# Kernel optimization log

Measured on AMD Instinct MI355X. Metric: run time of the kernel, lower is better.

The kernel has to match this reference:

```python
import jax, jax.numpy as jnp
import numpy as np
from jax import lax

EPS = 1e-5

def conv1x1(x, w, b=None):
    # x: [B,C,H,W], w: [O,C]
    y = jnp.einsum('bchw,oc->bohw', x, w)
    if b is not None:
        y = y + b[None, :, None, None]
    return y

def channel_attention(x, w1, w2):
    # x: [B,C,H,W]; w1: [C//r, C]; w2: [C, C//r]
    avg = jnp.mean(x, axis=(2, 3))                     # [B,C]
    h = jax.nn.relu(jnp.einsum('bc,rc->br', avg, w1))  # [B,C//r]
    s = jax.nn.sigmoid(jnp.einsum('br,cr->bc', h, w2)) # [B,C]
    return s[:, :, None, None]

def spatial_attention(x, w, b):
    # x: [B,C,H,W]; w: [1,2,7,7]
    avg = jnp.mean(x, axis=1, keepdims=True)
    mx = jnp.max(x, axis=1, keepdims=True)
    cat = jnp.concatenate([avg, mx], axis=1)           # [B,2,H,W]
    y = lax.conv_general_dilated(cat, w, (1, 1), 'SAME',
                                 dimension_numbers=('NCHW', 'OIHW', 'NCHW'))
    return jax.nn.sigmoid(y + b[None, :, None, None])

def cross_attention(x, y, q_w, q_b, k_w, k_b, v_w, v_b, gamma):
    B, C, H, W = x.shape
    HW = H * W
    q = conv1x1(x, q_w, q_b).reshape(B, -1, HW)        # [B,C8,HW]
    k = conv1x1(y, k_w, k_b).reshape(B, -1, HW)        # [B,C8,HW]
    v = conv1x1(y, v_w, v_b).reshape(B, C, HW)         # [B,C,HW]
    attn = jax.nn.softmax(jnp.einsum('bcn,bcm->bnm', q, k), axis=-1)  # [B,HW,HW]
    out = jnp.einsum('bcm,bnm->bcn', v, attn).reshape(B, C, H, W)
    return gamma * out + x

def batchnorm_relu(x, scale, bias):
    # train-mode BN: batch statistics over (N,H,W)
    mean = jnp.mean(x, axis=(0, 2, 3), keepdims=True)
    var = jnp.var(x, axis=(0, 2, 3), keepdims=True)
    xn = (x - mean) * lax.rsqrt(var + EPS)
    return jax.nn.relu(xn * scale[None, :, None, None] + bias[None, :, None, None])

def caf_forward(swin_feat, resnet_feat, proj_w, proj_b, ca_w1, ca_w2, sa_w, sa_b,
                q_w, q_b, k_w, k_b, v_w, v_b, gamma, refine_w, refine_b, bn_scale, bn_bias):
    s = conv1x1(swin_feat, proj_w, proj_b)
    r = conv1x1(resnet_feat, proj_w, proj_b)
    es = s * channel_attention(s, ca_w1, ca_w2) * spatial_attention(s, sa_w, sa_b)
    er = r * channel_attention(r, ca_w1, ca_w2) * spatial_attention(r, sa_w, sa_b)
    cross = cross_attention(es, er, q_w, q_b, k_w, k_b, v_w, v_b, gamma)
    cat = jnp.concatenate([cross, es], axis=1)         # [B, 2C, H, W]
    y = conv1x1(cat, refine_w, refine_b)
    return batchnorm_relu(y, bn_scale, bn_bias)

def setup_inputs() -> dict:
    key = jax.random.key(0)
    ks = jax.random.split(key, 16)
    B, Cin, H, W = 4, 128, 64, 64
    C = 64            # resnet_ch // 2
    R = C // 16       # channel attention reduction
    C8 = C // 8       # cross-attention qk dim
    sd = lambda fan_in: 1.0 / np.sqrt(fan_in)
    return {
        'swin_feat': jax.random.normal(ks[0], (B, Cin, H, W), jnp.float32),
        'resnet_feat': jax.random.normal(ks[1], (B, Cin, H, W), jnp.float32),
        'proj_w': jax.random.normal(ks[2], (C, Cin), jnp.float32) * sd(Cin),
        'proj_b': jnp.zeros((C,), jnp.float32),
        'ca_w1': jax.random.normal(ks[3], (R, C), jnp.float32) * sd(C),
        'ca_w2': jax.random.normal(ks[4], (C, R), jnp.float32) * sd(R),
        'sa_w': jax.random.normal(ks[5], (1, 2, 7, 7), jnp.float32) * sd(2 * 49),
        'sa_b': jnp.zeros((1,), jnp.float32),
        'q_w': jax.random.normal(ks[6], (C8, C), jnp.float32) * sd(C),
        'q_b': jnp.zeros((C8,), jnp.float32),
        'k_w': jax.random.normal(ks[7], (C8, C), jnp.float32) * sd(C),
        'k_b': jnp.zeros((C8,), jnp.float32),
        'v_w': jax.random.normal(ks[8], (C, C), jnp.float32) * sd(C),
        'v_b': jnp.zeros((C,), jnp.float32),
        'gamma': jnp.zeros((1,), jnp.float32),
        'refine_w': jax.random.normal(ks[9], (2 * C, 2 * C), jnp.float32) * sd(2 * C),
        'refine_b': jnp.zeros((2 * C,), jnp.float32),
        'bn_scale': jnp.ones((2 * C,), jnp.float32),
        'bn_bias': jnp.zeros((2 * C,), jnp.float32),
    }

def reference(swin_feat, resnet_feat, proj_w, proj_b, ca_w1, ca_w2, sa_w, sa_b,
              q_w, q_b, k_w, k_b, v_w, v_b, gamma, refine_w, refine_b, bn_scale, bn_bias):
    return caf_forward(swin_feat, resnet_feat, proj_w, proj_b, ca_w1, ca_w2, sa_w, sa_b,
                       q_w, q_b, k_w, k_b, v_w, v_b, gamma, refine_w, refine_b, bn_scale, bn_bias)
```

## Files before the change

### kernel.cpp

```cpp
#include <hip/hip_runtime.h>
#include <hip/hip_bf16.h>
#include <math.h>

#define NB   4
#define CIN  128
#define C    64
#define HH   64
#define WW   64
#define HW   4096
#define C8   8
#define RR   4
#define TWOC 128
#define LOG2E 1.44269504088896340736f

typedef __attribute__((ext_vector_type(8))) short short8;
typedef __attribute__((ext_vector_type(4))) float f32x4;
typedef __attribute__((ext_vector_type(16))) float f32x16;
typedef __attribute__((ext_vector_type(4))) int int4v;
typedef __attribute__((ext_vector_type(2))) unsigned uint2v;

__device__ inline ushort f2bf(float f) {
    union { float f; unsigned u; } x{ f };
    unsigned r = x.u + 0x7FFFu + ((x.u >> 16) & 1u);
    return (ushort)(r >> 16);
}

__device__ inline float fexp2(float x) { return __builtin_amdgcn_exp2f(x); }

__device__ inline short8 cvt8(f32x4 a, f32x4 b) {
    union { int i[4]; short8 s; } u;
    asm("v_cvt_pk_bf16_f32 %0, %1, %2" : "=v"(u.i[0]) : "v"(a[0]), "v"(a[1]));
    asm("v_cvt_pk_bf16_f32 %0, %1, %2" : "=v"(u.i[1]) : "v"(a[2]), "v"(a[3]));
    asm("v_cvt_pk_bf16_f32 %0, %1, %2" : "=v"(u.i[2]) : "v"(b[0]), "v"(b[1]));
    asm("v_cvt_pk_bf16_f32 %0, %1, %2" : "=v"(u.i[3]) : "v"(b[2]), "v"(b[3]));
    return u.s;
}

__global__ __launch_bounds__(256) void proj_gemm_kernel(
    const float* __restrict__ sw, const float* __restrict__ rn,
    const float* __restrict__ w, const float* __restrict__ bias,
    const float* __restrict__ gammap,
    float* __restrict__ s_t, float* __restrict__ r_t,
    float* __restrict__ part, float* __restrict__ avgc, float* __restrict__ maxc) {
    int bid = blockIdx.x;
    int hwT = bid & 63;
    int b   = (bid >> 6) & 3;
    int img = bid >> 8;
    if (img == 1 && gammap[0] == 0.f) return;
    int hw0 = hwT << 6;
    const float* x = (img ? rn : sw) + (size_t)b * CIN * HW + hw0;
    float* y = (img ? r_t : s_t) + (size_t)b * HW * C;

    __shared__ ushort xt[64 * 132];
    __shared__ float redc[4][64];
    int t = threadIdx.x;
    {
        int hwl = t & 63, cq = t >> 6;
        #pragma unroll
        for (int i = 0; i < 16; ++i) {
            int c = cq * 32 + i * 2;
            float a  = x[(size_t)c * HW + hwl];
            float b2 = x[(size_t)(c + 1) * HW + hwl];
            int pk;
            asm("v_cvt_pk_bf16_f32 %0, %1, %2" : "=v"(pk) : "v"(a), "v"(b2));
            *(unsigned*)&xt[hwl * 132 + c] = (unsigned)pk;
        }
    }
    __syncthreads();

    int lane = t & 63, wv = t >> 6;
    int colL = lane & 15, g = lane >> 4;
    int hwsub = wv << 4;
    f32x4 acc[4] = {};
    #pragma unroll
    for (int ks = 0; ks < 4; ++ks) {
        const ushort* ap = &xt[(hwsub + colL) * 132 + ks * 32 + g * 8];
        union { uint2 u2[2]; short8 s; } af;
        af.u2[0] = *(const uint2*)ap;
        af.u2[1] = *(const uint2*)(ap + 4);
        #pragma unroll
        for (int ot = 0; ot < 4; ++ot) {
            const float* wp = w + (size_t)(ot * 16 + colL) * CIN + ks * 32 + g * 8;
            short8 bf = cvt8(*(const f32x4*)wp, *(const f32x4*)(wp + 4));
            acc[ot] = __builtin_amdgcn_mfma_f32_16x16x32_bf16(af.s, bf, acc[ot], 0, 0, 0);
        }
    }

    float rowsum[4], rowmax[4], colsum[4];
    #pragma unroll
    for (int r = 0; r < 4; ++r) { rowsum[r] = 0.f; rowmax[r] = -1e30f; }
    #pragma unroll
    for (int ot = 0; ot < 4; ++ot) colsum[ot] = 0.f;
    #pragma unroll
    for (int ot = 0; ot < 4; ++ot) {
        float bb = bias[ot * 16 + colL];
        #pragma unroll
        for (int r = 0; r < 4; ++r) {
            float v = acc[ot][r] + bb;
            y[(size_t)(hw0 + hwsub + g * 4 + r) * C + ot * 16 + colL] = v;
            rowsum[r] += v;
            rowmax[r] = fmaxf(rowmax[r], v);
            colsum[ot] += v;
        }
    }
    #pragma unroll
    for (int d = 1; d < 16; d <<= 1) {
        #pragma unroll
        for (int r = 0; r < 4; ++r) {
            rowsum[r] += __shfl_xor(rowsum[r], d);
            rowmax[r] = fmaxf(rowmax[r], __shfl_xor(rowmax[r], d));
        }
    }
    if (colL == 0) {
        int ob = (img * 4 + b) * HW + hw0 + hwsub + g * 4;
        #pragma unroll
        for (int r = 0; r < 4; ++r) {
            avgc[ob + r] = rowsum[r] * (1.f / C);
            maxc[ob + r] = rowmax[r];
        }
    }
    #pragma unroll
    for (int d = 16; d < 64; d <<= 1) {
        #pragma unroll
        for (int ot = 0; ot < 4; ++ot) colsum[ot] += __shfl_xor(colsum[ot], d);
    }
    if (g == 0) {
        #pragma unroll
        for (int ot = 0; ot < 4; ++ot) redc[wv][ot * 16 + colL] = colsum[ot];
    }
    __syncthreads();
    if (t < 64)
        part[((size_t)(img * 4 + b) * 64 + hwT) * 64 + t] =
            redc[0][t] + redc[1][t] + redc[2][t] + redc[3][t];
}

__global__ __launch_bounds__(256) void casa_kernel(
    const float* __restrict__ part, const float* __restrict__ w1,
    const float* __restrict__ w2, float* __restrict__ cab,
    const float* __restrict__ avgc, const float* __restrict__ maxc,
    const float* __restrict__ saw, const float* __restrict__ bsa,
    const float* __restrict__ gammap, float* __restrict__ sab) {
    int bid = blockIdx.x;
    int t = threadIdx.x;
    if (bid == 128) {
        __shared__ float avs[8][64];
        __shared__ float hsh[8][RR];
        #pragma unroll
        for (int it = 0; it < 2; ++it) {
            int idx = t + it * 256;
            int c = idx & 63, ib = idx >> 6;
            float avg = 0.f;
            for (int hwT = 0; hwT < 64; ++hwT)
                avg += part[((size_t)ib * 64 + hwT) * 64 + c];
            avs[ib][c] = avg * (1.f / HW);
        }
        __syncthreads();
        if (t < 32) {
            int ib2 = t >> 2, r = t & 3;
            float a = 0.f;
            for (int cc = 0; cc < C; ++cc) a += avs[ib2][cc] * w1[r * C + cc];
            hsh[ib2][r] = fmaxf(a, 0.f);
        }
        __syncthreads();
        #pragma unroll
        for (int it = 0; it < 2; ++it) {
            int idx = t + it * 256;
            int c = idx & 63, ib = idx >> 6;
            float a = 0.f;
            #pragma unroll
            for (int r = 0; r < RR; ++r) a += hsh[ib][r] * w2[c * RR + r];
            cab[ib * 64 + c] = 1.f / (1.f + __expf(-a));
        }
        return;
    }
    int img = bid >> 6;
    if (img == 1 && gammap[0] == 0.f) return;
    __shared__ float wsh[98];
    if (t < 98) wsh[t] = saw[t];
    __syncthreads();
    int idx = (bid & 63) * 256 + t;
    int b = idx >> 12, hw = idx & 4095;
    int base = (img * 4 + b) * HW;
    int y0 = hw >> 6, x0 = hw & 63;
    float acc = bsa[0];
    for (int dy = -3; dy <= 3; ++dy) {
        int yy = y0 + dy; if (yy < 0 || yy >= HH) continue;
        for (int dx = -3; dx <= 3; ++dx) {
            int xx = x0 + dx; if (xx < 0 || xx >= WW) continue;
            int widx = (dy + 3) * 7 + (dx + 3);
            int p = base + yy * WW + xx;
            acc += avgc[p] * wsh[widx] + maxc[p] * wsh[49 + widx];
        }
    }
    sab[base + hw] = 1.f / (1.f + __expf(-acc));
}

__global__ __launch_bounds__(256) void vqk_proj_kernel(
    const float* __restrict__ es, const float* __restrict__ er,
    const float* __restrict__ vw, const float* __restrict__ vbv,
    const float* __restrict__ qw, const float* __restrict__ qbv,
    const float* __restrict__ kw, const float* __restrict__ kbv,
    const float* __restrict__ gammap,
    const float* __restrict__ cab, const float* __restrict__ sab,
    ushort* __restrict__ v_t, ushort* __restrict__ q_t, ushort* __restrict__ k_t) {
    if (gammap[0] == 0.f) return;
    __shared__ float wsh[64][64];
    __shared__ float qsh[8][64], ksh[8][64];
    int t = threadIdx.x;
    for (int i = t; i < 4096; i += 256) wsh[i >> 6][i & 63] = vw[i];
    for (int i = t; i < 512; i += 256) qsh[i >> 6][i & 63] = qw[i];
    for (int i = t; i < 512; i += 256) ksh[i >> 6][i & 63] = kw[i];
    __syncthreads();

    int bid = blockIdx.x;
    int hw = ((bid & 63) << 6) + (t & 63);
    int b  = bid >> 6;
    int qt = t >> 6;
    int c0 = qt << 4;
    const float* erp = er + (size_t)(b * HW + hw) * C;
    const float* esp = es + (size_t)(b * HW + hw) * C;
    const float* cas = cab + b * 64;
    const float* car = cab + (4 + b) * 64;
    float gs = sab[b * HW + hw];
    float gr = sab[(4 + b) * HW + hw];

    float va[16];
    #pragma unroll
    for (int j = 0; j < 16; ++j) va[j] = vbv[c0 + j];
    float qa[8], ka[8];
    #pragma unroll
    for (int o = 0; o < 8; ++o) { qa[o] = qbv[o]; ka[o] = kbv[o]; }

    #pragma unroll 4
    for (int i = 0; i < 16; ++i) {
        f32x4 xr = *(const f32x4*)(erp + i * 4) * *(const f32x4*)(car + i * 4) * gr;
        #pragma unroll
        for (int j = 0; j < 16; ++j) {
            const float* wr = &wsh[c0 + j][i * 4];
            va[j] += xr[0]*wr[0] + xr[1]*wr[1] + xr[2]*wr[2] + xr[3]*wr[3];
        }
        if (qt == 0) {
            f32x4 xs = *(const f32x4*)(esp + i * 4) * *(const f32x4*)(cas + i * 4) * gs;
            #pragma unroll
            for (int o = 0; o < 8; ++o) {
                const float* wr = &qsh[o][i * 4];
                qa[o] += xs[0]*wr[0] + xs[1]*wr[1] + xs[2]*wr[2] + xs[3]*wr[3];
            }
        } else if (qt == 3) {
            #pragma unroll
            for (int o = 0; o < 8; ++o) {
                const float* wr = &ksh[o][i * 4];
                ka[o] += xr[0]*wr[0] + xr[1]*wr[1] + xr[2]*wr[2] + xr[3]*wr[3];
            }
        }
    }

    #pragma unroll
    for (int j = 0; j < 16; ++j)
        v_t[((size_t)(b * C + c0 + j) << 12) + hw] = f2bf(va[j]);
    if (qt == 0) {
        union { ushort u[8]; int4v v; } qo;
        #pragma unroll
        for (int o = 0; o < 8; ++o) qo.u[o] = f2bf(qa[o] * LOG2E);
        *(int4v*)(q_t + (size_t)(b * HW + hw) * 8) = qo.v;
    } else if (qt == 3) {
        union { ushort u[8]; int4v v; } ko;
        #pragma unroll
        for (int o = 0; o < 8; ++o) ko.u[o] = f2bf(ka[o]);
        *(int4v*)(k_t + (size_t)(b * HW + hw) * 8) = ko.v;
    }
}

__global__ __launch_bounds__(512) void cross_attn_mfma(
    const ushort* __restrict__ q_t, const ushort* __restrict__ k_t,
    const ushort* __restrict__ v_t, const float* __restrict__ es_t,
    const float* __restrict__ gammap,
    const float* __restrict__ cab, const float* __restrict__ sab,
    float* __restrict__ cross_t)
{
    const float gma = gammap[0];
    if (gma == 0.f) return;
    const int tid  = threadIdx.x;
    const int lane = tid & 63;
    const int ws   = tid >> 6;
    const int b    = blockIdx.x >> 7;
    const int n0   = (blockIdx.x & 127) << 5;
    const int l31  = lane & 31;
    const int h    = lane >> 5;

    short8 qf = short8(0);
    if (lane < 32) qf = *(const short8*)(q_t + ((size_t)(b * HW) + n0 + l31) * 8);

    f32x16 acc0 = (f32x16)(0.f), acc1 = (f32x16)(0.f);
    float mrun = -1e30f, lrun = 0.f;

    const ushort* kbase = k_t + (size_t)(b * HW) * 8;
    const ushort* vb0 = v_t + ((size_t)(b * C) + l31) * HW + 8 * h;
    const ushort* vb1 = v_t + ((size_t)(b * C) + 32 + l31) * HW + 8 * h;

    const int mbeg = ws << 9, mend = mbeg + 512;
    for (int m0 = mbeg; m0 < mend; m0 += 32) {
        short8 kf = short8(0);
        if (lane < 32) kf = *(const short8*)(kbase + ((size_t)(m0 + l31)) * 8);
        short8 v00 = *(const short8*)(vb0 + m0);
        short8 v01 = *(const short8*)(vb0 + m0 + 16);
        short8 v10 = *(const short8*)(vb1 + m0);
        short8 v11 = *(const short8*)(vb1 + m0 + 16);

        f32x16 s = __builtin_amdgcn_mfma_f32_32x32x16_bf16(kf, qf, (f32x16)(0.f), 0, 0, 0);

        float t0 = fmaxf(fmaxf(s[0], s[1]), fmaxf(s[2], s[3]));
        float t1 = fmaxf(fmaxf(s[4], s[5]), fmaxf(s[6], s[7]));
        float t2 = fmaxf(fmaxf(s[8], s[9]), fmaxf(s[10], s[11]));
        float t3 = fmaxf(fmaxf(s[12], s[13]), fmaxf(s[14], s[15]));
        float tmax = fmaxf(fmaxf(t0, t1), fmaxf(t2, t3));
        tmax = fmaxf(tmax, __shfl_xor(tmax, 32));

        if (!__all(tmax <= mrun)) {
            float mnew = fmaxf(mrun, tmax);
            float corr = fexp2(mrun - mnew);
            lrun *= corr;
            acc0 *= corr;
            acc1 *= corr;
            mrun = mnew;
        }

        float p[16];
        #pragma unroll
        for (int r = 0; r < 16; ++r) p[r] = fexp2(s[r] - mrun);
        float ts = ((p[0]+p[1]) + (p[2]+p[3])) + ((p[4]+p[5]) + (p[6]+p[7]))
                 + ((p[8]+p[9]) + (p[10]+p[11])) + ((p[12]+p[13]) + (p[14]+p[15]));
        ts += __shfl_xor(ts, 32);
        lrun += ts;

        int c01, c23, c45, c67, c89, cAB, cCD, cEF;
        asm("v_cvt_pk_bf16_f32 %0, %1, %2" : "=v"(c01) : "v"(p[0]),  "v"(p[1]));
        asm("v_cvt_pk_bf16_f32 %0, %1, %2" : "=v"(c23) : "v"(p[2]),  "v"(p[3]));
        asm("v_cvt_pk_bf16_f32 %0, %1, %2" : "=v"(c45) : "v"(p[4]),  "v"(p[5]));
        asm("v_cvt_pk_bf16_f32 %0, %1, %2" : "=v"(c67) : "v"(p[6]),  "v"(p[7]));
        asm("v_cvt_pk_bf16_f32 %0, %1, %2" : "=v"(c89) : "v"(p[8]),  "v"(p[9]));
        asm("v_cvt_pk_bf16_f32 %0, %1, %2" : "=v"(cAB) : "v"(p[10]), "v"(p[11]));
        asm("v_cvt_pk_bf16_f32 %0, %1, %2" : "=v"(cCD) : "v"(p[12]), "v"(p[13]));
        asm("v_cvt_pk_bf16_f32 %0, %1, %2" : "=v"(cEF) : "v"(p[14]), "v"(p[15]));

        uint2v s1 = __builtin_amdgcn_permlane32_swap(c45, c01, false, false);
        uint2v s2 = __builtin_amdgcn_permlane32_swap(c67, c23, false, false);
        uint2v s3 = __builtin_amdgcn_permlane32_swap(cCD, c89, false, false);
        uint2v s4 = __builtin_amdgcn_permlane32_swap(cEF, cAB, false, false);

        union { unsigned u[4]; short8 s; } B0, B1;
        B0.u[0] = s1[1]; B0.u[1] = s2[1]; B0.u[2] = s1[0]; B0.u[3] = s2[0];
        B1.u[0] = s3[1]; B1.u[1] = s4[1]; B1.u[2] = s3[0]; B1.u[3] = s4[0];

        acc0 = __builtin_amdgcn_mfma_f32_32x32x16_bf16(v00, B0.s, acc0, 0, 0, 0);
        acc0 = __builtin_amdgcn_mfma_f32_32x32x16_bf16(v01, B1.s, acc0, 0, 0, 0);
        acc1 = __builtin_amdgcn_mfma_f32_32x32x16_bf16(v10, B0.s, acc1, 0, 0, 0);
        acc1 = __builtin_amdgcn_mfma_f32_32x32x16_bf16(v11, B1.s, acc1, 0, 0, 0);
    }

    __shared__ float paccs[8][64][33];
    __shared__ float pml[8][2][32];
    #pragma unroll
    for (int r = 0; r < 16; ++r) {
        int c = (r & 3) + 8 * (r >> 2) + 4 * h;
        paccs[ws][c][l31]      = acc0[r];
        paccs[ws][c + 32][l31] = acc1[r];
    }
    if (lane < 32) { pml[ws][0][l31] = mrun; pml[ws][1][l31] = lrun; }
    __syncthreads();

    #pragma unroll
    for (int k = 0; k < 4; ++k) {
        int c = tid & 63;
        int n = (tid >> 6) + 8 * k;
        float M = -1e30f;
        #pragma unroll
        for (int w2 = 0; w2 < 8; ++w2) M = fmaxf(M, pml[w2][0][n]);
        float L = 0.f, oacc = 0.f;
        #pragma unroll
        for (int w2 = 0; w2 < 8; ++w2) {
            float e = fexp2(pml[w2][0][n] - M);
            L += pml[w2][1][n] * e;
            oacc += paccs[w2][c][n] * e;
        }
        size_t idx = ((size_t)(b * HW) + n0 + n) * C + c;
        float esv = es_t[idx] * cab[b * 64 + c] * sab[b * HW + n0 + n];
        cross_t[idx] = gma * oacc / L + esv;
    }
}

__global__ __launch_bounds__(256) void refine_gemm_kernel(
    const float* __restrict__ cross_t, const float* __restrict__ es_t,
    const float* __restrict__ rw, const float* __restrict__ rb,
    const float* __restrict__ gammap,
    const float* __restrict__ cab, const float* __restrict__ sab,
    float* __restrict__ y, float* __restrict__ part2) {
    const bool g0 = (gammap[0] == 0.f);
    int bid = blockIdx.x;
    int hwT = bid & 63, b = bid >> 6;
    int hw0 = hwT << 6;
    int t = threadIdx.x, lane = t & 63, wv = t >> 6;
    int colL = lane & 15, g = lane >> 4;
    int hw = hw0 + wv * 16 + colL;
    const float* sp = es_t + ((size_t)(b * HW) + hw) * C;
    const float* cp = cross_t + ((size_t)(b * HW) + hw) * C;
    const float* cgb = cab + b * 64;
    float gate = sab[b * HW + hw];
    __shared__ float redp[4][128][2];
    f32x4 acc[8] = {};
    #pragma unroll
    for (int ks = 0; ks < 4; ++ks) {
        f32x4 x1, x2;
        if (ks < 2 && !g0) {
            const float* src = cp + (ks & 1) * 32 + g * 8;
            x1 = *(const f32x4*)src;
            x2 = *(const f32x4*)(src + 4);
        } else {
            const float* src = sp + (ks & 1) * 32 + g * 8;
            const float* cg = cgb + (ks & 1) * 32 + g * 8;
            x1 = *(const f32x4*)src * *(const f32x4*)cg * gate;
            x2 = *(const f32x4*)(src + 4) * *(const f32x4*)(cg + 4) * gate;
        }
        short8 bf = cvt8(x1, x2);
        #pragma unroll
        for (int ot = 0; ot < 8; ++ot) {
            const float* ap = rw + (size_t)(ot * 16 + colL) * TWOC + ks * 32 + g * 8;
            short8 afr = cvt8(*(const f32x4*)ap, *(const f32x4*)(ap + 4));
            acc[ot] = __builtin_amdgcn_mfma_f32_16x16x32_bf16(afr, bf, acc[ot], 0, 0, 0);
        }
    }
    #pragma unroll
    for (int ot = 0; ot < 8; ++ot) {
        int o = ot * 16 + g * 4;
        #pragma unroll
        for (int r = 0; r < 4; ++r) {
            float v = acc[ot][r] + rb[o + r];
            y[((size_t)(b * TWOC + o + r) << 12) + hw0 + wv * 16 + colL] = v;
            float vq = v * v;
            #pragma unroll
            for (int d = 1; d < 16; d <<= 1) {
                v  += __shfl_xor(v, d);
                vq += __shfl_xor(vq, d);
            }
            if (colL == 0) { redp[wv][o + r][0] = v; redp[wv][o + r][1] = vq; }
        }
    }
    __syncthreads();
    if (t < 128) {
        float s  = redp[0][t][0] + redp[1][t][0] + redp[2][t][0] + redp[3][t][0];
        float s2 = redp[0][t][1] + redp[1][t][1] + redp[2][t][1] + redp[3][t][1];
        part2[t * 256 + bid] = s;
        part2[32768 + t * 256 + bid] = s2;
    }
}

__global__ __launch_bounds__(256) void bn_apply_kernel(float* __restrict__ y,
                                const float* __restrict__ part2,
                                const float* __restrict__ sc,
                                const float* __restrict__ bi) {
    int blk = blockIdx.x;
    int t = threadIdx.x;
    int o = (blk >> 2) & 127;
    float s  = part2[o * 256 + t];
    float s2 = part2[32768 + o * 256 + t];
    for (int d = 32; d > 0; d >>= 1) { s += __shfl_down(s, d); s2 += __shfl_down(s2, d); }
    __shared__ float rs[4], rs2[4], bc[2];
    if ((t & 63) == 0) { rs[t >> 6] = s; rs2[t >> 6] = s2; }
    __syncthreads();
    if (t == 0) {
        float S  = rs[0] + rs[1] + rs[2] + rs[3];
        float S2 = rs2[0] + rs2[1] + rs2[2] + rs2[3];
        float m = S * (1.f / (NB * HW));
        float var = S2 * (1.f / (NB * HW)) - m * m;
        bc[0] = m;
        bc[1] = rsqrtf(var + 1e-5f);
    }
    __syncthreads();
    float m = bc[0], rstd = bc[1], scale = sc[o], bias = bi[o];
    int i4 = blk * 256 + t;
    f32x4 v = *(const f32x4*)&y[(size_t)i4 * 4];
    #pragma unroll
    for (int j = 0; j < 4; ++j) v[j] = fmaxf((v[j] - m) * rstd * scale + bias, 0.f);
    *(f32x4*)&y[(size_t)i4 * 4] = v;
}

extern "C" void kernel_launch(void* const* d_in, const int* in_sizes, int n_in,
                              void* d_out, int out_size, void* d_ws, size_t ws_size,
                              hipStream_t stream) {
    const float* swin   = (const float*)d_in[0];
    const float* resnet = (const float*)d_in[1];
    const float* proj_w = (const float*)d_in[2];
    const float* proj_b = (const float*)d_in[3];
    const float* ca_w1  = (const float*)d_in[4];
    const float* ca_w2  = (const float*)d_in[5];
    const float* sa_w   = (const float*)d_in[6];
    const float* sa_b   = (const float*)d_in[7];
    const float* q_w    = (const float*)d_in[8];
    const float* q_b    = (const float*)d_in[9];
    const float* k_w    = (const float*)d_in[10];
    const float* k_b    = (const float*)d_in[11];
    const float* v_w    = (const float*)d_in[12];
    const float* v_b    = (const float*)d_in[13];
    const float* gamma  = (const float*)d_in[14];
    const float* ref_w  = (const float*)d_in[15];
    const float* ref_b  = (const float*)d_in[16];
    const float* bn_sc  = (const float*)d_in[17];
    const float* bn_bi  = (const float*)d_in[18];
    float* out = (float*)d_out;

    float* ws = (float*)d_ws;
    float* s_t    = ws;
    float* r_t    = s_t + 1048576;
    float* cross_t= r_t + 1048576;
    float* part   = cross_t + 1048576;
    float* cab    = part + 32768;
    float* avgc   = cab + 512;
    float* maxc   = avgc + 32768;
    float* sab    = maxc + 32768;
    float* part2  = sab + 32768;
    ushort* q_t   = (ushort*)(part2 + 65536);
    ushort* k_t   = q_t + 131072;
    ushort* v_t   = k_t + 131072;

    proj_gemm_kernel<<<512, 256, 0, stream>>>(swin, resnet, proj_w, proj_b, gamma,
                                              s_t, r_t, part, avgc, maxc);
    casa_kernel<<<129, 256, 0, stream>>>(part, ca_w1, ca_w2, cab, avgc, maxc,
                                         sa_w, sa_b, gamma, sab);
    vqk_proj_kernel<<<256, 256, 0, stream>>>(s_t, r_t, v_w, v_b, q_w, q_b, k_w, k_b,
                                             gamma, cab, sab, v_t, q_t, k_t);
    cross_attn_mfma<<<NB * 128, 512, 0, stream>>>(q_t, k_t, v_t, s_t, gamma,
                                                  cab, sab, cross_t);
    refine_gemm_kernel<<<256, 256, 0, stream>>>(cross_t, s_t, ref_w, ref_b, gamma,
                                                cab, sab, out, part2);
    bn_apply_kernel<<<NB * TWOC * HW / 1024, 256, 0, stream>>>(out, part2, bn_sc, bn_bi);
}
```

Before: 49.28 us.

## Fuse all CAF stages into one cooperative persistent kernel with grid syncs

Replaces the six separate kernel launches (projection GEMM, channel/spatial attention, V/Q/K projection, cross attention, refine GEMM, BN apply) with a single cooperative kernel of 256 blocks x 512 threads. Stages are separated by grid.sync(), and each block takes on more work per stage: two projection tiles per block and two attention jobs. The aim is to remove per-launch overhead and inter-kernel gaps on a workload that is small, especially when gamma is zero and the attention path is skipped. In exchange, the whole grid must be co-resident, it pays the cost of each grid barrier, and a large shared-memory footprint may limit occupancy.

```diff
diff --git a/kernel.cpp b/kernel.cpp
--- a/kernel.cpp
+++ b/kernel.cpp
@@ -1,6 +1,9 @@
 #include <hip/hip_runtime.h>
+#include <hip/hip_cooperative_groups.h>
 #include <hip/hip_bf16.h>
 #include <math.h>
+
+namespace cg = cooperative_groups;
 
 #define NB   4
 #define CIN  128
@@ -12,6 +15,7 @@
 #define RR   4
 #define TWOC 128
 #define LOG2E 1.44269504088896340736f
+#define NBLK 256
 
 typedef __attribute__((ext_vector_type(8))) short short8;
 typedef __attribute__((ext_vector_type(4))) float f32x4;
@@ -36,478 +40,439 @@
     return u.s;
 }
 
-__global__ __launch_bounds__(256) void proj_gemm_kernel(
-    const float* __restrict__ sw, const float* __restrict__ rn,
-    const float* __restrict__ w, const float* __restrict__ bias,
-    const float* __restrict__ gammap,
-    float* __restrict__ s_t, float* __restrict__ r_t,
-    float* __restrict__ part, float* __restrict__ avgc, float* __restrict__ maxc) {
-    int bid = blockIdx.x;
-    int hwT = bid & 63;
-    int b   = (bid >> 6) & 3;
-    int img = bid >> 8;
-    if (img == 1 && gammap[0] == 0.f) return;
-    int hw0 = hwT << 6;
-    const float* x = (img ? rn : sw) + (size_t)b * CIN * HW + hw0;
-    float* y = (img ? r_t : s_t) + (size_t)b * HW * C;
-
-    __shared__ ushort xt[64 * 132];
-    __shared__ float redc[4][64];
-    int t = threadIdx.x;
+struct CafArgs {
+    const float *sw, *rn, *pw, *pb, *w1, *w2, *saw, *bsa;
+    const float *qw, *qbv, *kw, *kbv, *vw, *vbv, *gammap, *rw, *rb, *sc, *bi;
+    float *out, *s_t, *r_t, *cross_t, *part, *cab, *avgc, *maxc, *sab, *part2;
+    ushort *q_t, *k_t, *v_t;
+};
+
+__global__ __launch_bounds__(512) void caf_mega(CafArgs a)
+{
+    __shared__ __align__(16) char smem[69632];
+    cg::grid_group grid = cg::this_grid();
+    const int t = threadIdx.x;
+    const int bid = blockIdx.x;
+    const float gma = a.gammap[0];
+    const bool g0 = (gma == 0.f);
+
     {
-        int hwl = t & 63, cq = t >> 6;
-        #pragma unroll
-        for (int i = 0; i < 16; ++i) {
-            int c = cq * 32 + i * 2;
-            float a  = x[(size_t)c * HW + hwl];
-            float b2 = x[(size_t)(c + 1) * HW + hwl];
-            int pk;
-            asm("v_cvt_pk_bf16_f32 %0, %1, %2" : "=v"(pk) : "v"(a), "v"(b2));
-            *(unsigned*)&xt[hwl * 132 + c] = (unsigned)pk;
-        }
+        const int grp = t >> 8, tl = t & 255;
+        const int tile = grp * 256 + bid;
+        const int hwT = tile & 63, b = (tile >> 6) & 3, img = tile >> 8;
+        const bool active = !(g0 && img == 1);
+        ushort* xt  = (ushort*)(smem + grp * 17920);
+        float* redc = (float*)(smem + grp * 17920 + 16896);
+        const int hw0 = hwT << 6;
+        const float* x = (img ? a.rn : a.sw) + (size_t)b * CIN * HW + hw0;
+        float* y = (img ? a.r_t : a.s_t) + (size_t)b * HW * C;
+        if (active) {
+            int hwl = tl & 63, cq = tl >> 6;
+            #pragma unroll
+            for (int i = 0; i < 16; ++i) {
+                int c = cq * 32 + i * 2;
+                float v1 = x[(size_t)c * HW + hwl];
+                float v2 = x[(size_t)(c + 1) * HW + hwl];
+                int pk;
+                asm("v_cvt_pk_bf16_f32 %0, %1, %2" : "=v"(pk) : "v"(v1), "v"(v2));
+                *(unsigned*)&xt[hwl * 132 + c] = (unsigned)pk;
+            }
+        }
+        __syncthreads();
+        if (active) {
+            int lane = tl & 63, wv = tl >> 6;
+            int colL = lane & 15, g = lane >> 4;
+            int hwsub = wv << 4;
+            f32x4 acc[4] = {};
+            #pragma unroll
+            for (int ks = 0; ks < 4; ++ks) {
+                const ushort* ap = &xt[(hwsub + colL) * 132 + ks * 32 + g * 8];
+                union { uint2 u2[2]; short8 s; } af;
+                af.u2[0] = *(const uint2*)ap;
+                af.u2[1] = *(const uint2*)(ap + 4);
+                #pragma unroll
+                for (int ot = 0; ot < 4; ++ot) {
+                    const float* wp = a.pw + (size_t)(ot * 16 + colL) * CIN + ks * 32 + g * 8;
+                    short8 bf = cvt8(*(const f32x4*)wp, *(const f32x4*)(wp + 4));
+                    acc[ot] = __builtin_amdgcn_mfma_f32_16x16x32_bf16(af.s, bf, acc[ot], 0, 0, 0);
+                }
+            }
+            float rowsum[4], rowmax[4], colsum[4];
+            #pragma unroll
+            for (int r = 0; r < 4; ++r) { rowsum[r] = 0.f; rowmax[r] = -1e30f; }
+            #pragma unroll
+            for (int ot = 0; ot < 4; ++ot) colsum[ot] = 0.f;
+            #pragma unroll
+            for (int ot = 0; ot < 4; ++ot) {
+                float bb = a.pb[ot * 16 + colL];
+                #pragma unroll
+                for (int r = 0; r < 4; ++r) {
+                    float v = acc[ot][r] + bb;
+                    y[(size_t)(hw0 + hwsub + g * 4 + r) * C + ot * 16 + colL] = v;
+                    rowsum[r] += v;
+                    rowmax[r] = fmaxf(rowmax[r], v);
+                    colsum[ot] += v;
+                }
+            }
+            #pragma unroll
+            for (int d = 1; d < 16; d <<= 1) {
+                #pragma unroll
+                for (int r = 0; r < 4; ++r) {
+                    rowsum[r] += __shfl_xor(rowsum[r], d);
+                    rowmax[r] = fmaxf(rowmax[r], __shfl_xor(rowmax[r], d));
+                }
+            }
+            if (colL == 0) {
+                int ob = (img * 4 + b) * HW + hw0 + hwsub + g * 4;
+                #pragma unroll
+                for (int r = 0; r < 4; ++r) {
+                    a.avgc[ob + r] = rowsum[r] * (1.f / C);
+                    a.maxc[ob + r] = rowmax[r];
+                }
+            }
+            #pragma unroll
+            for (int d = 16; d < 64; d <<= 1) {
+                #pragma unroll
+                for (int ot = 0; ot < 4; ++ot) colsum[ot] += __shfl_xor(colsum[ot], d);
+            }
+            if (g == 0) {
+                #pragma unroll
+                for (int ot = 0; ot < 4; ++ot) redc[wv * 64 + ot * 16 + colL] = colsum[ot];
+            }
+        }
+        __syncthreads();
+        if (active && tl < 64)
+            a.part[((size_t)(img * 4 + b) * 64 + hwT) * 64 + tl] =
+                redc[tl] + redc[64 + tl] + redc[128 + tl] + redc[192 + tl];
     }
-    __syncthreads();
-
-    int lane = t & 63, wv = t >> 6;
-    int colL = lane & 15, g = lane >> 4;
-    int hwsub = wv << 4;
-    f32x4 acc[4] = {};
-    #pragma unroll
-    for (int ks = 0; ks < 4; ++ks) {
-        const ushort* ap = &xt[(hwsub + colL) * 132 + ks * 32 + g * 8];
-        union { uint2 u2[2]; short8 s; } af;
-        af.u2[0] = *(const uint2*)ap;
-        af.u2[1] = *(const uint2*)(ap + 4);
-        #pragma unroll
-        for (int ot = 0; ot < 4; ++ot) {
-            const float* wp = w + (size_t)(ot * 16 + colL) * CIN + ks * 32 + g * 8;
-            short8 bf = cvt8(*(const f32x4*)wp, *(const f32x4*)(wp + 4));
-            acc[ot] = __builtin_amdgcn_mfma_f32_16x16x32_bf16(af.s, bf, acc[ot], 0, 0, 0);
-        }
-    }
-
-    float rowsum[4], rowmax[4], colsum[4];
-    #pragma unroll
-    for (int r = 0; r < 4; ++r) { rowsum[r] = 0.f; rowmax[r] = -1e30f; }
-    #pragma unroll
-    for (int ot = 0; ot < 4; ++ot) colsum[ot] = 0.f;
-    #pragma unroll
-    for (int ot = 0; ot < 4; ++ot) {
-        float bb = bias[ot * 16 + colL];
-        #pragma unroll
-        for (int r = 0; r < 4; ++r) {
-            float v = acc[ot][r] + bb;
-            y[(size_t)(hw0 + hwsub + g * 4 + r) * C + ot * 16 + colL] = v;
-            rowsum[r] += v;
-            rowmax[r] = fmaxf(rowmax[r], v);
-            colsum[ot] += v;
-        }
-    }
-    #pragma unroll
-    for (int d = 1; d < 16; d <<= 1) {
-        #pragma unroll
-        for (int r = 0; r < 4; ++r) {
-            rowsum[r] += __shfl_xor(rowsum[r], d);
-            rowmax[r] = fmaxf(rowmax[r], __shfl_xor(rowmax[r], d));
-        }
-    }
-    if (colL == 0) {
-        int ob = (img * 4 + b) * HW + hw0 + hwsub + g * 4;
-        #pragma unroll
-        for (int r = 0; r < 4; ++r) {
-            avgc[ob + r] = rowsum[r] * (1.f / C);
-            maxc[ob + r] = rowmax[r];
-        }
-    }
-    #pragma unroll
-    for (int d = 16; d < 64; d <<= 1) {
-        #pragma unroll
-        for (int ot = 0; ot < 4; ++ot) colsum[ot] += __shfl_xor(colsum[ot], d);
-    }
-    if (g == 0) {
-        #pragma unroll
-        for (int ot = 0; ot < 4; ++ot) redc[wv][ot * 16 + colL] = colsum[ot];
-    }
-    __syncthreads();
-    if (t < 64)
-        part[((size_t)(img * 4 + b) * 64 + hwT) * 64 + t] =
-            redc[0][t] + redc[1][t] + redc[2][t] + redc[3][t];
-}
-
-__global__ __launch_bounds__(256) void casa_kernel(
-    const float* __restrict__ part, const float* __restrict__ w1,
-    const float* __restrict__ w2, float* __restrict__ cab,
-    const float* __restrict__ avgc, const float* __restrict__ maxc,
-    const float* __restrict__ saw, const float* __restrict__ bsa,
-    const float* __restrict__ gammap, float* __restrict__ sab) {
-    int bid = blockIdx.x;
-    int t = threadIdx.x;
-    if (bid == 128) {
-        __shared__ float avs[8][64];
-        __shared__ float hsh[8][RR];
-        #pragma unroll
-        for (int it = 0; it < 2; ++it) {
-            int idx = t + it * 256;
-            int c = idx & 63, ib = idx >> 6;
+    grid.sync();
+
+    if (bid == 64) {
+        float* avs = (float*)smem;
+        float* hsh = (float*)(smem + 2048);
+        {
+            int c = t & 63, ib = t >> 6;
             float avg = 0.f;
             for (int hwT = 0; hwT < 64; ++hwT)
-                avg += part[((size_t)ib * 64 + hwT) * 64 + c];
-            avs[ib][c] = avg * (1.f / HW);
+                avg += a.part[((size_t)ib * 64 + hwT) * 64 + c];
+            avs[ib * 64 + c] = avg * (1.f / HW);
         }
         __syncthreads();
         if (t < 32) {
             int ib2 = t >> 2, r = t & 3;
-            float a = 0.f;
-            for (int cc = 0; cc < C; ++cc) a += avs[ib2][cc] * w1[r * C + cc];
-            hsh[ib2][r] = fmaxf(a, 0.f);
+            float acc = 0.f;
+            for (int cc = 0; cc < C; ++cc) acc += avs[ib2 * 64 + cc] * a.w1[r * C + cc];
+            hsh[ib2 * 4 + r] = fmaxf(acc, 0.f);
         }
         __syncthreads();
+        {
+            int c = t & 63, ib = t >> 6;
+            float acc = 0.f;
+            #pragma unroll
+            for (int r = 0; r < RR; ++r) acc += hsh[ib * 4 + r] * a.w2[c * RR + r];
+            a.cab[ib * 64 + c] = 1.f / (1.f + __expf(-acc));
+        }
+    } else if (bid < 64) {
+        float* wsh = (float*)smem;
+        if (t < 98) wsh[t] = a.saw[t];
+        __syncthreads();
+        int idx = bid * 512 + t;
+        int ib = idx >> 12, hw = idx & 4095;
+        if (!(g0 && ib >= 4)) {
+            int base = ib * HW;
+            int y0 = hw >> 6, x0 = hw & 63;
+            float acc = a.bsa[0];
+            for (int dy = -3; dy <= 3; ++dy) {
+                int yy = y0 + dy; if (yy < 0 || yy >= HH) continue;
+                for (int dx = -3; dx <= 3; ++dx) {
+                    int xx = x0 + dx; if (xx < 0 || xx >= WW) continue;
+                    int widx = (dy + 3) * 7 + (dx + 3);
+                    int p = base + yy * WW + xx;
+                    acc += a.avgc[p] * wsh[widx] + a.maxc[p] * wsh[49 + widx];
+                }
+            }
+            a.sab[base + hw] = 1.f / (1.f + __expf(-acc));
+        }
+    }
+    grid.sync();
+
+    if (!g0) {
+        {
+            float* wshv = (float*)smem;
+            float* qsh = (float*)(smem + 16384);
+            float* ksh = (float*)(smem + 18432);
+            for (int i = t; i < 4096; i += 512) wshv[i] = a.vw[i];
+            if (t < 512) { qsh[t] = a.qw[t]; ksh[t] = a.kw[t]; }
+            __syncthreads();
+            if (t < 256) {
+                int hw = ((bid & 63) << 6) + (t & 63);
+                int b  = bid >> 6;
+                int qt = t >> 6;
+                int c0 = qt << 4;
+                const float* erp = a.r_t + (size_t)(b * HW + hw) * C;
+                const float* esp = a.s_t + (size_t)(b * HW + hw) * C;
+                const float* cas = a.cab + b * 64;
+                const float* car = a.cab + (4 + b) * 64;
+                float gs = a.sab[b * HW + hw];
+                float gr = a.sab[(4 + b) * HW + hw];
+                float va[16];
+                #pragma unroll
+                for (int j = 0; j < 16; ++j) va[j] = a.vbv[c0 + j];
+                float qa[8], ka[8];
+                #pragma unroll
+                for (int o = 0; o < 8; ++o) { qa[o] = a.qbv[o]; ka[o] = a.kbv[o]; }
+                #pragma unroll 4
+                for (int i = 0; i < 16; ++i) {
+                    f32x4 xr = *(const f32x4*)(erp + i * 4) * *(const f32x4*)(car + i * 4) * gr;
+                    #pragma unroll
+                    for (int j = 0; j < 16; ++j) {
+                        const float* wr = &wshv[(c0 + j) * 64 + i * 4];
+                        va[j] += xr[0]*wr[0] + xr[1]*wr[1] + xr[2]*wr[2] + xr[3]*wr[3];
+                    }
+                    if (qt == 0) {
+                        f32x4 xs = *(const f32x4*)(esp + i * 4) * *(const f32x4*)(cas + i * 4) * gs;
+                        #pragma unroll
+                        for (int o = 0; o < 8; ++o) {
+                            const float* wr = &qsh[o * 64 + i * 4];
+                            qa[o] += xs[0]*wr[0] + xs[1]*wr[1] + xs[2]*wr[2] + xs[3]*wr[3];
+                        }
+                    } else if (qt == 3) {
+                        #pragma unroll
+                        for (int o = 0; o < 8; ++o) {
+                            const float* wr = &ksh[o * 64 + i * 4];
+                            ka[o] += xr[0]*wr[0] + xr[1]*wr[1] + xr[2]*wr[2] + xr[3]*wr[3];
+                        }
+                    }
+                }
+                #pragma unroll
+                for (int j = 0; j < 16; ++j)
+                    a.v_t[((size_t)(b * C + c0 + j) << 12) + hw] = f2bf(va[j]);
+                if (qt == 0) {
+                    union { ushort u[8]; int4v v; } qo;
+                    #pragma unroll
+                    for (int o = 0; o < 8; ++o) qo.u[o] = f2bf(qa[o] * LOG2E);
+                    *(int4v*)(a.q_t + (size_t)(b * HW + hw) * 8) = qo.v;
+                } else if (qt == 3) {
+                    union { ushort u[8]; int4v v; } ko;
+                    #pragma unroll
+                    for (int o = 0; o < 8; ++o) ko.u[o] = f2bf(ka[o]);
+                    *(int4v*)(a.k_t + (size_t)(b * HW + hw) * 8) = ko.v;
+                }
+            }
+        }
+        grid.sync();
+
+        float* paccs = (float*)smem;
+        float* pml   = (float*)(smem + 67584);
+        for (int rep = 0; rep < 2; ++rep) {
+            int job = bid * 2 + rep;
+            const int lane = t & 63;
+            const int ws2  = t >> 6;
+            const int b    = job >> 7;
+            const int n0   = (job & 127) << 5;
+            const int l31  = lane & 31;
+            const int h    = lane >> 5;
+            short8 qf = short8(0);
+            if (lane < 32) qf = *(const short8*)(a.q_t + ((size_t)(b * HW) + n0 + l31) * 8);
+            f32x16 acc0 = (f32x16)(0.f), acc1 = (f32x16)(0.f);
+            float mrun = -1e30f, lrun = 0.f;
+            const ushort* kbase = a.k_t + (size_t)(b * HW) * 8;
+            const ushort* vb0 = a.v_t + ((size_t)(b * C) + l31) * HW + 8 * h;
+            const ushort* vb1 = a.v_t + ((size_t)(b * C) + 32 + l31) * HW + 8 * h;
+            const int mbeg = ws2 << 9, mend = mbeg + 512;
+            for (int m0 = mbeg; m0 < mend; m0 += 32) {
+                short8 kf = short8(0);
+                if (lane < 32) kf = *(const short8*)(kbase + ((size_t)(m0 + l31)) * 8);
+                short8 v00 = *(const short8*)(vb0 + m0);
+                short8 v01 = *(const short8*)(vb0 + m0 + 16);
+                short8 v10 = *(const short8*)(vb1 + m0);
+                short8 v11 = *(const short8*)(vb1 + m0 + 16);
+                f32x16 s = __builtin_amdgcn_mfma_f32_32x32x16_bf16(kf, qf, (f32x16)(0.f), 0, 0, 0);
+                float t0 = fmaxf(fmaxf(s[0], s[1]), fmaxf(s[2], s[3]));
+                float t1 = fmaxf(fmaxf(s[4], s[5]), fmaxf(s[6], s[7]));
+                float t2 = fmaxf(fmaxf(s[8], s[9]), fmaxf(s[10], s[11]));
+                float t3 = fmaxf(fmaxf(s[12], s[13]), fmaxf(s[14], s[15]));
+                float tmax = fmaxf(fmaxf(t0, t1), fmaxf(t2, t3));
+                tmax = fmaxf(tmax, __shfl_xor(tmax, 32));
+                if (!__all(tmax <= mrun)) {
+                    float mnew = fmaxf(mrun, tmax);
+                    float corr = fexp2(mrun - mnew);
+                    lrun *= corr;
+                    acc0 *= corr;
+                    acc1 *= corr;
+                    mrun = mnew;
+                }
+                float p[16];
+                #pragma unroll
+                for (int r = 0; r < 16; ++r) p[r] = fexp2(s[r] - mrun);
+                float ts = ((p[0]+p[1]) + (p[2]+p[3])) + ((p[4]+p[5]) + (p[6]+p[7]))
+                         + ((p[8]+p[9]) + (p[10]+p[11])) + ((p[12]+p[13]) + (p[14]+p[15]));
+                ts += __shfl_xor(ts, 32);
+                lrun += ts;
+                int c01, c23, c45, c67, c89, cAB, cCD, cEF;
+                asm("v_cvt_pk_bf16_f32 %0, %1, %2" : "=v"(c01) : "v"(p[0]),  "v"(p[1]));
+                asm("v_cvt_pk_bf16_f32 %0, %1, %2" : "=v"(c23) : "v"(p[2]),  "v"(p[3]));
+                asm("v_cvt_pk_bf16_f32 %0, %1, %2" : "=v"(c45) : "v"(p[4]),  "v"(p[5]));
+                asm("v_cvt_pk_bf16_f32 %0, %1, %2" : "=v"(c67) : "v"(p[6]),  "v"(p[7]));
+                asm("v_cvt_pk_bf16_f32 %0, %1, %2" : "=v"(c89) : "v"(p[8]),  "v"(p[9]));
+                asm("v_cvt_pk_bf16_f32 %0, %1, %2" : "=v"(cAB) : "v"(p[10]), "v"(p[11]));
+                asm("v_cvt_pk_bf16_f32 %0, %1, %2" : "=v"(cCD) : "v"(p[12]), "v"(p[13]));
+                asm("v_cvt_pk_bf16_f32 %0, %1, %2" : "=v"(cEF) : "v"(p[14]), "v"(p[15]));
+                uint2v s1 = __builtin_amdgcn_permlane32_swap(c45, c01, false, false);
+                uint2v s2 = __builtin_amdgcn_permlane32_swap(c67, c23, false, false);
+                uint2v s3 = __builtin_amdgcn_permlane32_swap(cCD, c89, false, false);
+                uint2v s4 = __builtin_amdgcn_permlane32_swap(cEF, cAB, false, false);
+                union { unsigned u[4]; short8 s; } B0, B1;
+                B0.u[0] = s1[1]; B0.u[1] = s2[1]; B0.u[2] = s1[0]; B0.u[3] = s2[0];
+                B1.u[0] = s3[1]; B1.u[1] = s4[1]; B1.u[2] = s3[0]; B1.u[3] = s4[0];
+                acc0 = __builtin_amdgcn_mfma_f32_32x32x16_bf16(v00, B0.s, acc0, 0, 0, 0);
+                acc0 = __builtin_amdgcn_mfma_f32_32x32x16_bf16(v01, B1.s, acc0, 0, 0, 0);
+                acc1 = __builtin_amdgcn_mfma_f32_32x32x16_bf16(v10, B0.s, acc1, 0, 0, 0);
+                acc1 = __builtin_amdgcn_mfma_f32_32x32x16_bf16(v11, B1.s, acc1, 0, 0, 0);
+            }
+            #pragma unroll
+            for (int r = 0; r < 16; ++r) {
+                int c = (r & 3) + 8 * (r >> 2) + 4 * h;
+                paccs[(ws2 * 64 + c) * 33 + l31]        = acc0[r];
+                paccs[(ws2 * 64 + c + 32) * 33 + l31]   = acc1[r];
+            }
+            if (lane < 32) { pml[(ws2 * 2 + 0) * 32 + l31] = mrun; pml[(ws2 * 2 + 1) * 32 + l31] = lrun; }
+            __syncthreads();
+            #pragma unroll
+            for (int k = 0; k < 4; ++k) {
+                int c = t & 63;
+                int n = (t >> 6) + 8 * k;
+                float M = -1e30f;
+                #pragma unroll
+                for (int w3 = 0; w3 < 8; ++w3) M = fmaxf(M, pml[(w3 * 2) * 32 + n]);
+                float L = 0.f, oacc = 0.f;
+                #pragma unroll
+                for (int w3 = 0; w3 < 8; ++w3) {
+                    float e = fexp2(pml[(w3 * 2) * 32 + n] - M);
+                    L += pml[(w3 * 2 + 1) * 32 + n] * e;
+                    oacc += paccs[(w3 * 64 + c) * 33 + n] * e;
+                }
+                size_t idx = ((size_t)(b * HW) + n0 + n) * C + c;
+                float esv = a.s_t[idx] * a.cab[b * 64 + c] * a.sab[b * HW + n0 + n];
+                a.cross_t[idx] = gma * oacc / L + esv;
+            }
+            __syncthreads();
+        }
+        grid.sync();
+    }
+
+    {
+        int hwT = bid & 63, b = bid >> 6;
+        int hw0 = hwT << 6;
+        int lane = t & 63, wv = t >> 6;
+        int colL = lane & 15, g = lane >> 4;
+        int wh = wv & 3, oh = wv >> 2;
+        int hw = hw0 + wh * 16 + colL;
+        const float* sp = a.s_t + ((size_t)(b * HW) + hw) * C;
+        const float* cp = a.cross_t + ((size_t)(b * HW) + hw) * C;
+        const float* cgb = a.cab + b * 64;
+        float gate = a.sab[b * HW + hw];
+        float* redp = (float*)smem;
+        f32x4 acc[4] = {};
         #pragma unroll
-        for (int it = 0; it < 2; ++it) {
-            int idx = t + it * 256;
-            int c = idx & 63, ib = idx >> 6;
-            float a = 0.f;
-            #pragma unroll
-            for (int r = 0; r < RR; ++r) a += hsh[ib][r] * w2[c * RR + r];
-            cab[ib * 64 + c] = 1.f / (1.f + __expf(-a));
-        }
-        return;
+        for (int ks = 0; ks < 4; ++ks) {
+            f32x4 x1, x2;
+            if (ks < 2 && !g0) {
+                const float* src = cp + (ks & 1) * 32 + g * 8;
+                x1 = *(const f32x4*)src;
+                x2 = *(const f32x4*)(src + 4);
+            } else {
+                const float* src = sp + (ks & 1) * 32 + g * 8;
+                const float* cg = cgb + (ks & 1) * 32 + g * 8;
+                x1 = *(const f32x4*)src * *(const f32x4*)cg * gate;
+                x2 = *(const f32x4*)(src + 4) * *(const f32x4*)(cg + 4) * gate;
+            }
+            short8 bf = cvt8(x1, x2);
+            #pragma unroll
+            for (int ot2 = 0; ot2 < 4; ++ot2) {
+                int ot = oh * 4 + ot2;
+                const float* ap = a.rw + (size_t)(ot * 16 + colL) * TWOC + ks * 32 + g * 8;
+                short8 afr = cvt8(*(const f32x4*)ap, *(const f32x4*)(ap + 4));
+                acc[ot2] = __builtin_amdgcn_mfma_f32_16x16x32_bf16(afr, bf, acc[ot2], 0, 0, 0);
+            }
+        }
+        #pragma unroll
+        for (int ot2 = 0; ot2 < 4; ++ot2) {
+            int ot = oh * 4 + ot2;
+            int o = ot * 16 + g * 4;
+            #pragma unroll
+            for (int r = 0; r < 4; ++r) {
+                float v = acc[ot2][r] + a.rb[o + r];
+                a.out[((size_t)(b * TWOC + o + r) << 12) + hw] = v;
+                float vq = v * v;
+                #pragma unroll
+                for (int d = 1; d < 16; d <<= 1) {
+                    v  += __shfl_xor(v, d);
+                    vq += __shfl_xor(vq, d);
+                }
+                if (colL == 0) {
+                    int ol = ot2 * 16 + g * 4 + r;
+                    redp[(wv * 64 + ol) * 2 + 0] = v;
+                    redp[(wv * 64 + ol) * 2 + 1] = vq;
+                }
+            }
+        }
+        __syncthreads();
+        if (t < 128) {
+            int o = t;
+            int ohh = o >> 6, ol = o & 63;
+            float s = 0.f, s2 = 0.f;
+            #pragma unroll
+            for (int w3 = 0; w3 < 4; ++w3) {
+                int wvi = ohh * 4 + w3;
+                s  += redp[(wvi * 64 + ol) * 2 + 0];
+                s2 += redp[(wvi * 64 + ol) * 2 + 1];
+            }
+            a.part2[o * 256 + bid] = s;
+            a.part2[32768 + o * 256 + bid] = s2;
+        }
     }
-    int img = bid >> 6;
-    if (img == 1 && gammap[0] == 0.f) return;
-    __shared__ float wsh[98];
-    if (t < 98) wsh[t] = saw[t];
-    __syncthreads();
-    int idx = (bid & 63) * 256 + t;
-    int b = idx >> 12, hw = idx & 4095;
-    int base = (img * 4 + b) * HW;
-    int y0 = hw >> 6, x0 = hw & 63;
-    float acc = bsa[0];
-    for (int dy = -3; dy <= 3; ++dy) {
-        int yy = y0 + dy; if (yy < 0 || yy >= HH) continue;
-        for (int dx = -3; dx <= 3; ++dx) {
-            int xx = x0 + dx; if (xx < 0 || xx >= WW) continue;
-            int widx = (dy + 3) * 7 + (dx + 3);
-            int p = base + yy * WW + xx;
-            acc += avgc[p] * wsh[widx] + maxc[p] * wsh[49 + widx];
+    grid.sync();
+
+    {
+        float* rs  = (float*)smem;
+        float* rs2 = rs + 8;
+        float* bc  = rs2 + 8;
+        f32x4* y4 = (f32x4*)a.out;
+        for (int rep = 0; rep < 2; ++rep) {
+            int bo = bid * 2 + rep;
+            int o = bo & 127;
+            float s = 0.f, s2 = 0.f;
+            if (t < 256) { s = a.part2[o * 256 + t]; s2 = a.part2[32768 + o * 256 + t]; }
+            for (int d = 32; d > 0; d >>= 1) { s += __shfl_down(s, d); s2 += __shfl_down(s2, d); }
+            if ((t & 63) == 0) { rs[t >> 6] = s; rs2[t >> 6] = s2; }
+            __syncthreads();
+            if (t == 0) {
+                float S  = rs[0] + rs[1] + rs[2] + rs[3];
+                float S2 = rs2[0] + rs2[1] + rs2[2] + rs2[3];
+                float m = S * (1.f / (NB * HW));
+                float var = S2 * (1.f / (NB * HW)) - m * m;
+                bc[0] = m;
+                bc[1] = rsqrtf(var + 1e-5f);
+            }
+            __syncthreads();
+            float m = bc[0], rstd = bc[1], scale = a.sc[o], bias = a.bi[o];
+            #pragma unroll
+            for (int k = 0; k < 2; ++k) {
+                size_t i4 = (size_t)bo * 1024 + t + k * 512;
+                f32x4 v = y4[i4];
+                #pragma unroll
+                for (int j = 0; j < 4; ++j) v[j] = fmaxf((v[j] - m) * rstd * scale + bias, 0.f);
+                y4[i4] = v;
+            }
+            __syncthreads();
         }
     }
-    sab[base + hw] = 1.f / (1.f + __expf(-acc));
-}
-
-__global__ __launch_bounds__(256) void vqk_proj_kernel(
-    const float* __restrict__ es, const float* __restrict__ er,
-    const float* __restrict__ vw, const float* __restrict__ vbv,
-    const float* __restrict__ qw, const float* __restrict__ qbv,
-    const float* __restrict__ kw, const float* __restrict__ kbv,
-    const float* __restrict__ gammap,
-    const float* __restrict__ cab, const float* __restrict__ sab,
-    ushort* __restrict__ v_t, ushort* __restrict__ q_t, ushort* __restrict__ k_t) {
-    if (gammap[0] == 0.f) return;
-    __shared__ float wsh[64][64];
-    __shared__ float qsh[8][64], ksh[8][64];
-    int t = threadIdx.x;
-    for (int i = t; i < 4096; i += 256) wsh[i >> 6][i & 63] = vw[i];
-    for (int i = t; i < 512; i += 256) qsh[i >> 6][i & 63] = qw[i];
-    for (int i = t; i < 512; i += 256) ksh[i >> 6][i & 63] = kw[i];
-    __syncthreads();
-
-    int bid = blockIdx.x;
-    int hw = ((bid & 63) << 6) + (t & 63);
-    int b  = bid >> 6;
-    int qt = t >> 6;
-    int c0 = qt << 4;
-    const float* erp = er + (size_t)(b * HW + hw) * C;
-    const float* esp = es + (size_t)(b * HW + hw) * C;
-    const float* cas = cab + b * 64;
-    const float* car = cab + (4 + b) * 64;
-    float gs = sab[b * HW + hw];
-    float gr = sab[(4 + b) * HW + hw];
-
-    float va[16];
-    #pragma unroll
-    for (int j = 0; j < 16; ++j) va[j] = vbv[c0 + j];
-    float qa[8], ka[8];
-    #pragma unroll
-    for (int o = 0; o < 8; ++o) { qa[o] = qbv[o]; ka[o] = kbv[o]; }
-
-    #pragma unroll 4
-    for (int i = 0; i < 16; ++i) {
-        f32x4 xr = *(const f32x4*)(erp + i * 4) * *(const f32x4*)(car + i * 4) * gr;
-        #pragma unroll
-        for (int j = 0; j < 16; ++j) {
-            const float* wr = &wsh[c0 + j][i * 4];
-            va[j] += xr[0]*wr[0] + xr[1]*wr[1] + xr[2]*wr[2] + xr[3]*wr[3];
-        }
-        if (qt == 0) {
-            f32x4 xs = *(const f32x4*)(esp + i * 4) * *(const f32x4*)(cas + i * 4) * gs;
-            #pragma unroll
-            for (int o = 0; o < 8; ++o) {
-                const float* wr = &qsh[o][i * 4];
-                qa[o] += xs[0]*wr[0] + xs[1]*wr[1] + xs[2]*wr[2] + xs[3]*wr[3];
-            }
-        } else if (qt == 3) {
-            #pragma unroll
-            for (int o = 0; o < 8; ++o) {
-                const float* wr = &ksh[o][i * 4];
-                ka[o] += xr[0]*wr[0] + xr[1]*wr[1] + xr[2]*wr[2] + xr[3]*wr[3];
-            }
-        }
-    }
-
-    #pragma unroll
-    for (int j = 0; j < 16; ++j)
-        v_t[((size_t)(b * C + c0 + j) << 12) + hw] = f2bf(va[j]);
-    if (qt == 0) {
-        union { ushort u[8]; int4v v; } qo;
-        #pragma unroll
-        for (int o = 0; o < 8; ++o) qo.u[o] = f2bf(qa[o] * LOG2E);
-        *(int4v*)(q_t + (size_t)(b * HW + hw) * 8) = qo.v;
-    } else if (qt == 3) {
-        union { ushort u[8]; int4v v; } ko;
-        #pragma unroll
-        for (int o = 0; o < 8; ++o) ko.u[o] = f2bf(ka[o]);
-        *(int4v*)(k_t + (size_t)(b * HW + hw) * 8) = ko.v;
-    }
-}
-
-__global__ __launch_bounds__(512) void cross_attn_mfma(
-    const ushort* __restrict__ q_t, const ushort* __restrict__ k_t,
-    const ushort* __restrict__ v_t, const float* __restrict__ es_t,
-    const float* __restrict__ gammap,
-    const float* __restrict__ cab, const float* __restrict__ sab,
-    float* __restrict__ cross_t)
-{
-    const float gma = gammap[0];
-    if (gma == 0.f) return;
-    const int tid  = threadIdx.x;
-    const int lane = tid & 63;
-    const int ws   = tid >> 6;
-    const int b    = blockIdx.x >> 7;
-    const int n0   = (blockIdx.x & 127) << 5;
-    const int l31  = lane & 31;
-    const int h    = lane >> 5;
-
-    short8 qf = short8(0);
-    if (lane < 32) qf = *(const short8*)(q_t + ((size_t)(b * HW) + n0 + l31) * 8);
-
-    f32x16 acc0 = (f32x16)(0.f), acc1 = (f32x16)(0.f);
-    float mrun = -1e30f, lrun = 0.f;
-
-    const ushort* kbase = k_t + (size_t)(b * HW) * 8;
-    const ushort* vb0 = v_t + ((size_t)(b * C) + l31) * HW + 8 * h;
-    const ushort* vb1 = v_t + ((size_t)(b * C) + 32 + l31) * HW + 8 * h;
-
-    const int mbeg = ws << 9, mend = mbeg + 512;
-    for (int m0 = mbeg; m0 < mend; m0 += 32) {
-        short8 kf = short8(0);
-        if (lane < 32) kf = *(const short8*)(kbase + ((size_t)(m0 + l31)) * 8);
-        short8 v00 = *(const short8*)(vb0 + m0);
-        short8 v01 = *(const short8*)(vb0 + m0 + 16);
-        short8 v10 = *(const short8*)(vb1 + m0);
-        short8 v11 = *(const short8*)(vb1 + m0 + 16);
-
-        f32x16 s = __builtin_amdgcn_mfma_f32_32x32x16_bf16(kf, qf, (f32x16)(0.f), 0, 0, 0);
-
-        float t0 = fmaxf(fmaxf(s[0], s[1]), fmaxf(s[2], s[3]));
-        float t1 = fmaxf(fmaxf(s[4], s[5]), fmaxf(s[6], s[7]));
-        float t2 = fmaxf(fmaxf(s[8], s[9]), fmaxf(s[10], s[11]));
-        float t3 = fmaxf(fmaxf(s[12], s[13]), fmaxf(s[14], s[15]));
-        float tmax = fmaxf(fmaxf(t0, t1), fmaxf(t2, t3));
-        tmax = fmaxf(tmax, __shfl_xor(tmax, 32));
-
-        if (!__all(tmax <= mrun)) {
-            float mnew = fmaxf(mrun, tmax);
-            float corr = fexp2(mrun - mnew);
-            lrun *= corr;
-            acc0 *= corr;
-            acc1 *= corr;
-            mrun = mnew;
-        }
-
-        float p[16];
-        #pragma unroll
-        for (int r = 0; r < 16; ++r) p[r] = fexp2(s[r] - mrun);
-        float ts = ((p[0]+p[1]) + (p[2]+p[3])) + ((p[4]+p[5]) + (p[6]+p[7]))
-                 + ((p[8]+p[9]) + (p[10]+p[11])) + ((p[12]+p[13]) + (p[14]+p[15]));
-        ts += __shfl_xor(ts, 32);
-        lrun += ts;
-
-        int c01, c23, c45, c67, c89, cAB, cCD, cEF;
-        asm("v_cvt_pk_bf16_f32 %0, %1, %2" : "=v"(c01) : "v"(p[0]),  "v"(p[1]));
-        asm("v_cvt_pk_bf16_f32 %0, %1, %2" : "=v"(c23) : "v"(p[2]),  "v"(p[3]));
-        asm("v_cvt_pk_bf16_f32 %0, %1, %2" : "=v"(c45) : "v"(p[4]),  "v"(p[5]));
-        asm("v_cvt_pk_bf16_f32 %0, %1, %2" : "=v"(c67) : "v"(p[6]),  "v"(p[7]));
-        asm("v_cvt_pk_bf16_f32 %0, %1, %2" : "=v"(c89) : "v"(p[8]),  "v"(p[9]));
-        asm("v_cvt_pk_bf16_f32 %0, %1, %2" : "=v"(cAB) : "v"(p[10]), "v"(p[11]));
-        asm("v_cvt_pk_bf16_f32 %0, %1, %2" : "=v"(cCD) : "v"(p[12]), "v"(p[13]));
-        asm("v_cvt_pk_bf16_f32 %0, %1, %2" : "=v"(cEF) : "v"(p[14]), "v"(p[15]));
-
-        uint2v s1 = __builtin_amdgcn_permlane32_swap(c45, c01, false, false);
-        uint2v s2 = __builtin_amdgcn_permlane32_swap(c67, c23, false, false);
-        uint2v s3 = __builtin_amdgcn_permlane32_swap(cCD, c89, false, false);
-        uint2v s4 = __builtin_amdgcn_permlane32_swap(cEF, cAB, false, false);
-
-        union { unsigned u[4]; short8 s; } B0, B1;
-        B0.u[0] = s1[1]; B0.u[1] = s2[1]; B0.u[2] = s1[0]; B0.u[3] = s2[0];
-        B1.u[0] = s3[1]; B1.u[1] = s4[1]; B1.u[2] = s3[0]; B1.u[3] = s4[0];
-
-        acc0 = __builtin_amdgcn_mfma_f32_32x32x16_bf16(v00, B0.s, acc0, 0, 0, 0);
-        acc0 = __builtin_amdgcn_mfma_f32_32x32x16_bf16(v01, B1.s, acc0, 0, 0, 0);
-        acc1 = __builtin_amdgcn_mfma_f32_32x32x16_bf16(v10, B0.s, acc1, 0, 0, 0);
-        acc1 = __builtin_amdgcn_mfma_f32_32x32x16_bf16(v11, B1.s, acc1, 0, 0, 0);
-    }
-
-    __shared__ float paccs[8][64][33];
-    __shared__ float pml[8][2][32];
-    #pragma unroll
-    for (int r = 0; r < 16; ++r) {
-        int c = (r & 3) + 8 * (r >> 2) + 4 * h;
-        paccs[ws][c][l31]      = acc0[r];
-        paccs[ws][c + 32][l31] = acc1[r];
-    }
-    if (lane < 32) { pml[ws][0][l31] = mrun; pml[ws][1][l31] = lrun; }
-    __syncthreads();
-
-    #pragma unroll
-    for (int k = 0; k < 4; ++k) {
-        int c = tid & 63;
-        int n = (tid >> 6) + 8 * k;
-        float M = -1e30f;
-        #pragma unroll
-        for (int w2 = 0; w2 < 8; ++w2) M = fmaxf(M, pml[w2][0][n]);
-        float L = 0.f, oacc = 0.f;
-        #pragma unroll
-        for (int w2 = 0; w2 < 8; ++w2) {
-            float e = fexp2(pml[w2][0][n] - M);
-            L += pml[w2][1][n] * e;
-            oacc += paccs[w2][c][n] * e;
-        }
-        size_t idx = ((size_t)(b * HW) + n0 + n) * C + c;
-        float esv = es_t[idx] * cab[b * 64 + c] * sab[b * HW + n0 + n];
-        cross_t[idx] = gma * oacc / L + esv;
-    }
-}
-
-__global__ __launch_bounds__(256) void refine_gemm_kernel(
-    const float* __restrict__ cross_t, const float* __restrict__ es_t,
-    const float* __restrict__ rw, const float* __restrict__ rb,
-    const float* __restrict__ gammap,
-    const float* __restrict__ cab, const float* __restrict__ sab,
-    float* __restrict__ y, float* __restrict__ part2) {
-    const bool g0 = (gammap[0] == 0.f);
-    int bid = blockIdx.x;
-    int hwT = bid & 63, b = bid >> 6;
-    int hw0 = hwT << 6;
-    int t = threadIdx.x, lane = t & 63, wv = t >> 6;
-    int colL = lane & 15, g = lane >> 4;
-    int hw = hw0 + wv * 16 + colL;
-    const float* sp = es_t + ((size_t)(b * HW) + hw) * C;
-    const float* cp = cross_t + ((size_t)(b * HW) + hw) * C;
-    const float* cgb = cab + b * 64;
-    float gate = sab[b * HW + hw];
-    __shared__ float redp[4][128][2];
-    f32x4 acc[8] = {};
-    #pragma unroll
-    for (int ks = 0; ks < 4; ++ks) {
-        f32x4 x1, x2;
-        if (ks < 2 && !g0) {
-            const float* src = cp + (ks & 1) * 32 + g * 8;
-            x1 = *(const f32x4*)src;
-            x2 = *(const f32x4*)(src + 4);
-        } else {
-            const float* src = sp + (ks & 1) * 32 + g * 8;
-            const float* cg = cgb + (ks & 1) * 32 + g * 8;
-            x1 = *(const f32x4*)src * *(const f32x4*)cg * gate;
-            x2 = *(const f32x4*)(src + 4) * *(const f32x4*)(cg + 4) * gate;
-        }
-        short8 bf = cvt8(x1, x2);
-        #pragma unroll
-        for (int ot = 0; ot < 8; ++ot) {
-            const float* ap = rw + (size_t)(ot * 16 + colL) * TWOC + ks * 32 + g * 8;
-            short8 afr = cvt8(*(const f32x4*)ap, *(const f32x4*)(ap + 4));
-            acc[ot] = __builtin_amdgcn_mfma_f32_16x16x32_bf16(afr, bf, acc[ot], 0, 0, 0);
-        }
-    }
-    #pragma unroll
-    for (int ot = 0; ot < 8; ++ot) {
-        int o = ot * 16 + g * 4;
-        #pragma unroll
-        for (int r = 0; r < 4; ++r) {
-            float v = acc[ot][r] + rb[o + r];
-            y[((size_t)(b * TWOC + o + r) << 12) + hw0 + wv * 16 + colL] = v;
-            float vq = v * v;
-            #pragma unroll
-            for (int d = 1; d < 16; d <<= 1) {
-                v  += __shfl_xor(v, d);
-                vq += __shfl_xor(vq, d);
-            }
-            if (colL == 0) { redp[wv][o + r][0] = v; redp[wv][o + r][1] = vq; }
-        }
-    }
-    __syncthreads();
-    if (t < 128) {
-        float s  = redp[0][t][0] + redp[1][t][0] + redp[2][t][0] + redp[3][t][0];
-        float s2 = redp[0][t][1] + redp[1][t][1] + redp[2][t][1] + redp[3][t][1];
-        part2[t * 256 + bid] = s;
-        part2[32768 + t * 256 + bid] = s2;
-    }
-}
-
-__global__ __launch_bounds__(256) void bn_apply_kernel(float* __restrict__ y,
-                                const float* __restrict__ part2,
-                                const float* __restrict__ sc,
-                                const float* __restrict__ bi) {
-    int blk = blockIdx.x;
-    int t = threadIdx.x;
-    int o = (blk >> 2) & 127;
-    float s  = part2[o * 256 + t];
-    float s2 = part2[32768 + o * 256 + t];
-    for (int d = 32; d > 0; d >>= 1) { s += __shfl_down(s, d); s2 += __shfl_down(s2, d); }
-    __shared__ float rs[4], rs2[4], bc[2];
-    if ((t & 63) == 0) { rs[t >> 6] = s; rs2[t >> 6] = s2; }
-    __syncthreads();
-    if (t == 0) {
-        float S  = rs[0] + rs[1] + rs[2] + rs[3];
-        float S2 = rs2[0] + rs2[1] + rs2[2] + rs2[3];
-        float m = S * (1.f / (NB * HW));
-        float var = S2 * (1.f / (NB * HW)) - m * m;
-        bc[0] = m;
-        bc[1] = rsqrtf(var + 1e-5f);
-    }
-    __syncthreads();
-    float m = bc[0], rstd = bc[1], scale = sc[o], bias = bi[o];
-    int i4 = blk * 256 + t;
-    f32x4 v = *(const f32x4*)&y[(size_t)i4 * 4];
-    #pragma unroll
-    for (int j = 0; j < 4; ++j) v[j] = fmaxf((v[j] - m) * rstd * scale + bias, 0.f);
-    *(f32x4*)&y[(size_t)i4 * 4] = v;
 }
 
 extern "C" void kernel_launch(void* const* d_in, const int* in_sizes, int n_in,
                               void* d_out, int out_size, void* d_ws, size_t ws_size,
                               hipStream_t stream) {
-    const float* swin   = (const float*)d_in[0];
-    const float* resnet = (const float*)d_in[1];
-    const float* proj_w = (const float*)d_in[2];
-    const float* proj_b = (const float*)d_in[3];
-    const float* ca_w1  = (const float*)d_in[4];
-    const float* ca_w2  = (const float*)d_in[5];
-    const float* sa_w   = (const float*)d_in[6];
-    const float* sa_b   = (const float*)d_in[7];
-    const float* q_w    = (const float*)d_in[8];
-    const float* q_b    = (const float*)d_in[9];
-    const float* k_w    = (const float*)d_in[10];
-    const float* k_b    = (const float*)d_in[11];
-    const float* v_w    = (const float*)d_in[12];
-    const float* v_b    = (const float*)d_in[13];
-    const float* gamma  = (const float*)d_in[14];
-    const float* ref_w  = (const float*)d_in[15];
-    const float* ref_b  = (const float*)d_in[16];
-    const float* bn_sc  = (const float*)d_in[17];
-    const float* bn_bi  = (const float*)d_in[18];
-    float* out = (float*)d_out;
-
     float* ws = (float*)d_ws;
     float* s_t    = ws;
     float* r_t    = s_t + 1048576;
@@ -522,15 +487,23 @@
     ushort* k_t   = q_t + 131072;
     ushort* v_t   = k_t + 131072;
 
-    proj_gemm_kernel<<<512, 256, 0, stream>>>(swin, resnet, proj_w, proj_b, gamma,
-                                              s_t, r_t, part, avgc, maxc);
-    casa_kernel<<<129, 256, 0, stream>>>(part, ca_w1, ca_w2, cab, avgc, maxc,
-                                         sa_w, sa_b, gamma, sab);
-    vqk_proj_kernel<<<256, 256, 0, stream>>>(s_t, r_t, v_w, v_b, q_w, q_b, k_w, k_b,
-                                             gamma, cab, sab, v_t, q_t, k_t);
-    cross_attn_mfma<<<NB * 128, 512, 0, stream>>>(q_t, k_t, v_t, s_t, gamma,
-                                                  cab, sab, cross_t);
-    refine_gemm_kernel<<<256, 256, 0, stream>>>(cross_t, s_t, ref_w, ref_b, gamma,
-                                                cab, sab, out, part2);
-    bn_apply_kernel<<<NB * TWOC * HW / 1024, 256, 0, stream>>>(out, part2, bn_sc, bn_bi);
+    CafArgs a;
+    a.sw  = (const float*)d_in[0];  a.rn  = (const float*)d_in[1];
+    a.pw  = (const float*)d_in[2];  a.pb  = (const float*)d_in[3];
+    a.w1  = (const float*)d_in[4];  a.w2  = (const float*)d_in[5];
+    a.saw = (const float*)d_in[6];  a.bsa = (const float*)d_in[7];
+    a.qw  = (const float*)d_in[8];  a.qbv = (const float*)d_in[9];
+    a.kw  = (const float*)d_in[10]; a.kbv = (const float*)d_in[11];
+    a.vw  = (const float*)d_in[12]; a.vbv = (const float*)d_in[13];
+    a.gammap = (const float*)d_in[14];
+    a.rw  = (const float*)d_in[15]; a.rb  = (const float*)d_in[16];
+    a.sc  = (const float*)d_in[17]; a.bi  = (const float*)d_in[18];
+    a.out = (float*)d_out;
+    a.s_t = s_t; a.r_t = r_t; a.cross_t = cross_t;
+    a.part = part; a.cab = cab; a.avgc = avgc; a.maxc = maxc; a.sab = sab;
+    a.part2 = part2; a.q_t = q_t; a.k_t = k_t; a.v_t = v_t;
+
+    void* kp[] = { (void*)&a };
+    (void)hipLaunchCooperativeKernel((const void*)caf_mega, dim3(NBLK), dim3(512),
+                                     kp, 0, stream);
 }
```

After: 139.1 us. 182% more time.
